# Optimization experiments

Measured on AMD Instinct MI355X. Metric: run time of the kernel, lower is better.

The kernel has to match this reference:

```python
import jax, jax.numpy as jnp
import numpy as np

BATCH, L, E = 8192, 4096, 12  # E = log2(L) butterfly stages


def setup_inputs() -> dict:
    key = jax.random.key(0)
    kx, kw = jax.random.split(key)
    x = jax.random.normal(kx, (BATCH, L), dtype=jnp.float32)
    # Stacked per-stage weights: stage s has an (L, 2) coefficient table
    # (matches nn.Parameter(torch.randn(L, 2)) for each of E stages).
    W = jax.random.normal(kw, (E, L, 2), dtype=jnp.float32)
    return {"x": x, "W": W}


def _butterfly(x, W):
    # rightmost=True: apply the smallest-stride factor first (stride 1 -> L/2).
    B = x.shape[0]
    e = W.shape[0]
    y = x
    for s in range(e):
        d = 1 << s                      # pairing stride at this stage
        g = L // (2 * d)                # number of butterfly groups
        yr = y.reshape(B, g, 2, d)      # pairs (i, i ^ d) along last dim
        Wr = W[s].reshape(g, 2, d, 2)   # per-row 2x2 mix coefficients
        top, bot = yr[:, :, 0, :], yr[:, :, 1, :]
        new_top = Wr[:, 0, :, 0] * top + Wr[:, 0, :, 1] * bot
        new_bot = Wr[:, 1, :, 0] * bot + Wr[:, 1, :, 1] * top
        y = jnp.stack([new_top, new_bot], axis=2).reshape(B, L)
    return y


def reference(x, W):
    return _butterfly(x, W)
```

## Files before the change

### kernel.cpp

```cpp
#include <hip/hip_runtime.h>


constexpr int LROW = 4096;
constexpr int RPB  = 4;
constexpr int NBLK = 8192 / RPB;

__device__ __forceinline__ int slotf(int P3, int P2, int P1, int P0) {
    const int b012 = (P0 ^ P1 ^ P2) & 7;
    const int b3   = (P1 ^ (P2 >> 1)) & 1;
    const int U    = (P3 << 5) | (P2 << 2) | (P1 >> 1);
    return (U << 4) | (b3 << 3) | b012;
}

template<int S>
__device__ __forceinline__ void loadA(float2 (&w)[8], const float* __restrict__ W, int t) {
    const float4* q4 = reinterpret_cast<const float4*>(W + (size_t)S * 8192 + 16 * t);
    #pragma unroll
    for (int m = 0; m < 4; ++m) {
        const float4 q = q4[m];
        w[2*m]   = make_float2(q.x, q.y);
        w[2*m+1] = make_float2(q.z, q.w);
    }
}

template<int S, int STEP>
__device__ __forceinline__ void loadG(float2 (&w)[8], const float* __restrict__ W, int pbase) {
    const float2* q2 = reinterpret_cast<const float2*>(W) + (size_t)S * 4096 + pbase;
    #pragma unroll
    for (int m = 0; m < 8; ++m) w[m] = q2[m * STEP];
}

template<int DL>
__device__ __forceinline__ void stage(float (&v)[RPB][8], const float2 (&w)[8]) {
    #pragma unroll
    for (int g = 0; g < 8; g += 2*DL)
        #pragma unroll
        for (int m = 0; m < DL; ++m) {
            const int a = g + m, c = a + DL;
            #pragma unroll
            for (int r = 0; r < RPB; ++r) {
                const float va = v[r][a], vb = v[r][c];
                v[r][a] = w[a].x * va + w[a].y * vb;
                v[r][c] = w[c].x * vb + w[c].y * va;
            }
        }
}

__global__ __launch_bounds__(512)
void butterfly12_kernel(const float* __restrict__ x,
                        const float* __restrict__ W,
                        float* __restrict__ out)
{
    __shared__ float2 lds[6144];

    const int t  = threadIdx.x;
    const int t6 = t >> 6;
    const int t3 = (t >> 3) & 7;
    const int t0 = t & 7;
    const size_t row0 = (size_t)blockIdx.x * RPB;

    float v[RPB][8];
    float2 wbA[8], wbB[8];

    #pragma unroll
    for (int r = 0; r < RPB; ++r) {
        const float4* xr = reinterpret_cast<const float4*>(x + (row0 + r) * LROW + 8 * t);
        const float4 qa = xr[0], qb = xr[1];
        v[r][0]=qa.x; v[r][1]=qa.y; v[r][2]=qa.z; v[r][3]=qa.w;
        v[r][4]=qb.x; v[r][5]=qb.y; v[r][6]=qb.z; v[r][7]=qb.w;
    }

    const int pB = t6*512 + t3*64 + t0;
    const int pC = t6*512 + t3*8  + t0;

    loadA<0>(wbA, W, t);
    loadA<1>(wbB, W, t);
    stage<1>(v, wbA);
    loadA<2>(wbA, W, t);
    stage<2>(v, wbB);
    loadG<3, 8>(wbB, W, pB);
    stage<4>(v, wbA);

    #pragma unroll
    for (int h = 0; h < 2; ++h) {
        asm volatile("" ::: "memory");
        #pragma unroll
        for (int i = 0; i < 8; ++i)
            lds[slotf(t6, t3, t0, i)] = make_float2(v[2*h][i], v[2*h+1][i]);
        asm volatile("s_waitcnt lgkmcnt(0)" ::: "memory");
        __builtin_amdgcn_sched_barrier(0);
        #pragma unroll
        for (int j = 0; j < 8; ++j) {
            const float2 q = lds[slotf(t6, t3, j, t0)];
            v[2*h][j] = q.x; v[2*h+1][j] = q.y;
        }
    }

    loadG<4, 8>(wbA, W, pB);
    stage<1>(v, wbB);
    loadG<5, 8>(wbB, W, pB);
    stage<2>(v, wbA);
    loadG<6, 64>(wbA, W, pC);
    stage<4>(v, wbB);

    #pragma unroll
    for (int h = 0; h < 2; ++h) {
        asm volatile("" ::: "memory");
        #pragma unroll
        for (int j = 0; j < 8; ++j)
            lds[slotf(t6, t3, j, t0)] = make_float2(v[2*h][j], v[2*h+1][j]);
        asm volatile("s_waitcnt lgkmcnt(0)" ::: "memory");
        __builtin_amdgcn_sched_barrier(0);
        #pragma unroll
        for (int k = 0; k < 8; ++k) {
            const float2 q = lds[slotf(t6, k, t3, t0)];
            v[2*h][k] = q.x; v[2*h+1][k] = q.y;
        }
    }

    loadG<7, 64>(wbB, W, pC);
    stage<1>(v, wbA);
    loadG<8, 64>(wbA, W, pC);
    stage<2>(v, wbB);
    loadG<9, 512>(wbB, W, t);
    stage<4>(v, wbA);

    {
        #pragma unroll
        for (int k = 0; k < 8; ++k)
            lds[slotf(t6, k, t3, t0)] = make_float2(v[0][k], v[1][k]);
        __syncthreads();
        #pragma unroll
        for (int m = 0; m < 8; ++m) {
            const float2 q = lds[slotf(m, t6, t3, t0)];
            v[0][m] = q.x; v[1][m] = q.y;
        }
        __syncthreads();
        #pragma unroll
        for (int k = 0; k < 8; ++k)
            lds[slotf(t6, k, t3, t0)] = make_float2(v[2][k], v[3][k]);
        __syncthreads();
        #pragma unroll
        for (int m = 0; m < 8; ++m) {
            const float2 q = lds[slotf(m, t6, t3, t0)];
            v[2][m] = q.x; v[3][m] = q.y;
        }
    }

    loadG<10, 512>(wbA, W, t);
    stage<1>(v, wbB);
    loadG<11, 512>(wbB, W, t);
    stage<2>(v, wbA);
    stage<4>(v, wbB);

    #pragma unroll
    for (int r = 0; r < RPB; ++r) {
        float* orow = out + (row0 + r) * LROW;
        #pragma unroll
        for (int m = 0; m < 8; ++m)
            orow[m*512 + t] = v[r][m];
    }
}

extern "C" void kernel_launch(void* const* d_in, const int* in_sizes, int n_in,
                              void* d_out, int out_size, void* d_ws, size_t ws_size,
                              hipStream_t stream) {
    const float* x = (const float*)d_in[0];
    const float* W = (const float*)d_in[1];
    float* out = (float*)d_out;

    butterfly12_kernel<<<NBLK, 512, 0, stream>>>(x, W, out);
}
```

Measured before the change: 268.3 us.

## Process four row groups per block with software-prefetched next-group loads

Each block now handles four groups of four rows sequentially, prefetching the next group's x rows into a second register set while computing the current group. The block count drops by a factor of four. The double-buffered weight loads are replaced by per-stage scoped loads. A __syncthreads is added before LDS reuse across groups. This is meant to hide global load latency behind compute, but it raises register pressure (two v arrays) and reduces the number of blocks and so the parallelism across CUs.

```diff
diff --git a/kernel.cpp b/kernel.cpp
--- a/kernel.cpp
+++ b/kernel.cpp
@@ -3,7 +3,8 @@
 
 constexpr int LROW = 4096;
 constexpr int RPB  = 4;
-constexpr int NBLK = 8192 / RPB;
+constexpr int GPB  = 4;
+constexpr int NBLK = 8192 / (RPB * GPB);
 
 __device__ __forceinline__ int slotf(int P3, int P2, int P1, int P0) {
     const int b012 = (P0 ^ P1 ^ P2) & 7;
@@ -46,22 +47,8 @@
         }
 }
 
-__global__ __launch_bounds__(512)
-void butterfly12_kernel(const float* __restrict__ x,
-                        const float* __restrict__ W,
-                        float* __restrict__ out)
-{
-    __shared__ float2 lds[6144];
-
-    const int t  = threadIdx.x;
-    const int t6 = t >> 6;
-    const int t3 = (t >> 3) & 7;
-    const int t0 = t & 7;
-    const size_t row0 = (size_t)blockIdx.x * RPB;
-
-    float v[RPB][8];
-    float2 wbA[8], wbB[8];
-
+__device__ __forceinline__ void loadX(float (&v)[RPB][8], const float* __restrict__ x,
+                                      size_t row0, int t) {
     #pragma unroll
     for (int r = 0; r < RPB; ++r) {
         const float4* xr = reinterpret_cast<const float4*>(x + (row0 + r) * LROW + 8 * t);
@@ -69,17 +56,27 @@
         v[r][0]=qa.x; v[r][1]=qa.y; v[r][2]=qa.z; v[r][3]=qa.w;
         v[r][4]=qb.x; v[r][5]=qb.y; v[r][6]=qb.z; v[r][7]=qb.w;
     }
+}
+
+template<bool PF>
+__device__ __forceinline__ void group_body(float (&v)[RPB][8], float (&vn)[RPB][8],
+                                           const float* __restrict__ x,
+                                           const float* __restrict__ W,
+                                           float* __restrict__ out,
+                                           size_t row0, size_t row0n,
+                                           int t, int t6, int t3, int t0,
+                                           float2* lds)
+{
+    if (PF) loadX(vn, x, row0n, t);
 
     const int pB = t6*512 + t3*64 + t0;
     const int pC = t6*512 + t3*8  + t0;
 
-    loadA<0>(wbA, W, t);
-    loadA<1>(wbB, W, t);
-    stage<1>(v, wbA);
-    loadA<2>(wbA, W, t);
-    stage<2>(v, wbB);
-    loadG<3, 8>(wbB, W, pB);
-    stage<4>(v, wbA);
+    { float2 w[8]; loadA<0>(w, W, t); stage<1>(v, w); }
+    { float2 w[8]; loadA<1>(w, W, t); stage<2>(v, w); }
+    { float2 w[8]; loadA<2>(w, W, t); stage<4>(v, w); }
+
+    __syncthreads();
 
     #pragma unroll
     for (int h = 0; h < 2; ++h) {
@@ -96,12 +93,9 @@
         }
     }
 
-    loadG<4, 8>(wbA, W, pB);
-    stage<1>(v, wbB);
-    loadG<5, 8>(wbB, W, pB);
-    stage<2>(v, wbA);
-    loadG<6, 64>(wbA, W, pC);
-    stage<4>(v, wbB);
+    { float2 w[8]; loadG<3, 8>(w, W, pB); stage<1>(v, w); }
+    { float2 w[8]; loadG<4, 8>(w, W, pB); stage<2>(v, w); }
+    { float2 w[8]; loadG<5, 8>(w, W, pB); stage<4>(v, w); }
 
     #pragma unroll
     for (int h = 0; h < 2; ++h) {
@@ -118,12 +112,9 @@
         }
     }
 
-    loadG<7, 64>(wbB, W, pC);
-    stage<1>(v, wbA);
-    loadG<8, 64>(wbA, W, pC);
-    stage<2>(v, wbB);
-    loadG<9, 512>(wbB, W, t);
-    stage<4>(v, wbA);
+    { float2 w[8]; loadG<6, 64>(w, W, pC); stage<1>(v, w); }
+    { float2 w[8]; loadG<7, 64>(w, W, pC); stage<2>(v, w); }
+    { float2 w[8]; loadG<8, 64>(w, W, pC); stage<4>(v, w); }
 
     {
         #pragma unroll
@@ -147,11 +138,9 @@
         }
     }
 
-    loadG<10, 512>(wbA, W, t);
-    stage<1>(v, wbB);
-    loadG<11, 512>(wbB, W, t);
-    stage<2>(v, wbA);
-    stage<4>(v, wbB);
+    { float2 w[8]; loadG<9,  512>(w, W, t); stage<1>(v, w); }
+    { float2 w[8]; loadG<10, 512>(w, W, t); stage<2>(v, w); }
+    { float2 w[8]; loadG<11, 512>(w, W, t); stage<4>(v, w); }
 
     #pragma unroll
     for (int r = 0; r < RPB; ++r) {
@@ -160,6 +149,29 @@
         for (int m = 0; m < 8; ++m)
             orow[m*512 + t] = v[r][m];
     }
+}
+
+__global__ __launch_bounds__(512)
+void butterfly12_kernel(const float* __restrict__ x,
+                        const float* __restrict__ W,
+                        float* __restrict__ out)
+{
+    __shared__ float2 lds[8192];
+
+    const int t  = threadIdx.x;
+    const int t6 = t >> 6;
+    const int t3 = (t >> 3) & 7;
+    const int t0 = t & 7;
+    const size_t rowbase = (size_t)blockIdx.x * (RPB * GPB);
+
+    float vA[RPB][8], vB[RPB][8];
+
+    loadX(vA, x, rowbase, t);
+
+    group_body<true >(vA, vB, x, W, out, rowbase + 0*RPB, rowbase + 1*RPB, t, t6, t3, t0, lds);
+    group_body<true >(vB, vA, x, W, out, rowbase + 1*RPB, rowbase + 2*RPB, t, t6, t3, t0, lds);
+    group_body<true >(vA, vB, x, W, out, rowbase + 2*RPB, rowbase + 3*RPB, t, t6, t3, t0, lds);
+    group_body<false>(vB, vA, x, W, out, rowbase + 3*RPB, rowbase + 3*RPB, t, t6, t3, t0, lds);
 }
 
 extern "C" void kernel_launch(void* const* d_in, const int* in_sizes, int n_in,
```

Measured after the change: 278.6 us. +3.8%, slower.

## Replace LDS transposes for middle stages with cross-lane swizzle exchanges

Applied to the files above, without the earlier changes.

Stages 3-8 now exchange partner values between lanes of the same wavefront using ds_swizzle (strides 1-16) and ds_bpermute (stride 32), replacing two LDS round-trip transposes. A single swizzled float4 LDS transpose, guarded by one barrier, redistributes data for the last three stages. The aim is to cut LDS traffic and barriers and to use coalesced weight loads. In exchange, every element now costs a cross-lane op at each of six stages and the multiply work roughly doubles, because each lane computes its own output.

```diff
diff --git a/kernel.cpp b/kernel.cpp
--- a/kernel.cpp
+++ b/kernel.cpp
@@ -5,11 +5,19 @@
 constexpr int RPB  = 4;
 constexpr int NBLK = 8192 / RPB;
 
-__device__ __forceinline__ int slotf(int P3, int P2, int P1, int P0) {
-    const int b012 = (P0 ^ P1 ^ P2) & 7;
-    const int b3   = (P1 ^ (P2 >> 1)) & 1;
-    const int U    = (P3 << 5) | (P2 << 2) | (P1 >> 1);
-    return (U << 4) | (b3 << 3) | b012;
+__device__ __forceinline__ int swz(int s) { return s ^ ((s >> 6) & 7); }
+
+template<int D>
+__device__ __forceinline__ float xl(float x, int bpa) {
+    const int xi = __builtin_bit_cast(int, x);
+    int r;
+    if      constexpr (D == 1)  r = __builtin_amdgcn_ds_swizzle(xi, 0x041F);
+    else if constexpr (D == 2)  r = __builtin_amdgcn_ds_swizzle(xi, 0x081F);
+    else if constexpr (D == 4)  r = __builtin_amdgcn_ds_swizzle(xi, 0x101F);
+    else if constexpr (D == 8)  r = __builtin_amdgcn_ds_swizzle(xi, 0x201F);
+    else if constexpr (D == 16) r = __builtin_amdgcn_ds_swizzle(xi, 0x401F);
+    else                        r = __builtin_amdgcn_ds_bpermute(bpa, xi);
+    return __builtin_bit_cast(float, r);
 }
 
 template<int S>
@@ -23,15 +31,15 @@
     }
 }
 
-template<int S, int STEP>
-__device__ __forceinline__ void loadG(float2 (&w)[8], const float* __restrict__ W, int pbase) {
-    const float2* q2 = reinterpret_cast<const float2*>(W) + (size_t)S * 4096 + pbase;
+template<int S>
+__device__ __forceinline__ void loadD(float2 (&w)[8], const float* __restrict__ W, int t) {
+    const float2* q2 = reinterpret_cast<const float2*>(W) + (size_t)S * 4096 + t;
     #pragma unroll
-    for (int m = 0; m < 8; ++m) w[m] = q2[m * STEP];
+    for (int m = 0; m < 8; ++m) w[m] = q2[m * 512];
 }
 
 template<int DL>
-__device__ __forceinline__ void stage(float (&v)[RPB][8], const float2 (&w)[8]) {
+__device__ __forceinline__ void rstage(float (&v)[RPB][8], const float2 (&w)[8]) {
     #pragma unroll
     for (int g = 0; g < 8; g += 2*DL)
         #pragma unroll
@@ -46,21 +54,33 @@
         }
 }
 
+template<int S, int D>
+__device__ __forceinline__ void xstage(float (&v)[RPB][8], const float* __restrict__ W,
+                                       int t, int bpa) {
+    float2 w[8];
+    loadA<S>(w, W, t);
+    #pragma unroll
+    for (int r = 0; r < RPB; ++r) {
+        float u[8];
+        #pragma unroll
+        for (int i = 0; i < 8; ++i) u[i] = xl<D>(v[r][i], bpa);
+        #pragma unroll
+        for (int i = 0; i < 8; ++i) v[r][i] = w[i].x * v[r][i] + w[i].y * u[i];
+    }
+}
+
 __global__ __launch_bounds__(512)
 void butterfly12_kernel(const float* __restrict__ x,
                         const float* __restrict__ W,
                         float* __restrict__ out)
 {
-    __shared__ float2 lds[6144];
+    __shared__ float4 lds4[4096];
 
-    const int t  = threadIdx.x;
-    const int t6 = t >> 6;
-    const int t3 = (t >> 3) & 7;
-    const int t0 = t & 7;
+    const int t   = threadIdx.x;
+    const int bpa = ((t & 63) ^ 32) << 2;
     const size_t row0 = (size_t)blockIdx.x * RPB;
 
     float v[RPB][8];
-    float2 wbA[8], wbB[8];
 
     #pragma unroll
     for (int r = 0; r < RPB; ++r) {
@@ -70,95 +90,37 @@
         v[r][4]=qb.x; v[r][5]=qb.y; v[r][6]=qb.z; v[r][7]=qb.w;
     }
 
-    const int pB = t6*512 + t3*64 + t0;
-    const int pC = t6*512 + t3*8  + t0;
+    { float2 w[8]; loadA<0>(w, W, t); rstage<1>(v, w); }
+    { float2 w[8]; loadA<1>(w, W, t); rstage<2>(v, w); }
+    { float2 w[8]; loadA<2>(w, W, t); rstage<4>(v, w); }
 
-    loadA<0>(wbA, W, t);
-    loadA<1>(wbB, W, t);
-    stage<1>(v, wbA);
-    loadA<2>(wbA, W, t);
-    stage<2>(v, wbB);
-    loadG<3, 8>(wbB, W, pB);
-    stage<4>(v, wbA);
+    xstage<3, 1 >(v, W, t, bpa);
+    xstage<4, 2 >(v, W, t, bpa);
+    xstage<5, 4 >(v, W, t, bpa);
+    xstage<6, 8 >(v, W, t, bpa);
+    xstage<7, 16>(v, W, t, bpa);
+    xstage<8, 32>(v, W, t, bpa);
 
     #pragma unroll
-    for (int h = 0; h < 2; ++h) {
-        asm volatile("" ::: "memory");
-        #pragma unroll
-        for (int i = 0; i < 8; ++i)
-            lds[slotf(t6, t3, t0, i)] = make_float2(v[2*h][i], v[2*h+1][i]);
-        asm volatile("s_waitcnt lgkmcnt(0)" ::: "memory");
-        __builtin_amdgcn_sched_barrier(0);
-        #pragma unroll
-        for (int j = 0; j < 8; ++j) {
-            const float2 q = lds[slotf(t6, t3, j, t0)];
-            v[2*h][j] = q.x; v[2*h+1][j] = q.y;
-        }
+    for (int i = 0; i < 8; ++i)
+        lds4[swz(8*t + i)] = make_float4(v[0][i], v[1][i], v[2][i], v[3][i]);
+    __syncthreads();
+    #pragma unroll
+    for (int k = 0; k < 8; ++k) {
+        const float4 q = lds4[swz(512*k + t)];
+        v[0][k] = q.x; v[1][k] = q.y; v[2][k] = q.z; v[3][k] = q.w;
     }
 
-    loadG<4, 8>(wbA, W, pB);
-    stage<1>(v, wbB);
-    loadG<5, 8>(wbB, W, pB);
-    stage<2>(v, wbA);
-    loadG<6, 64>(wbA, W, pC);
-    stage<4>(v, wbB);
-
-    #pragma unroll
-    for (int h = 0; h < 2; ++h) {
-        asm volatile("" ::: "memory");
-        #pragma unroll
-        for (int j = 0; j < 8; ++j)
-            lds[slotf(t6, t3, j, t0)] = make_float2(v[2*h][j], v[2*h+1][j]);
-        asm volatile("s_waitcnt lgkmcnt(0)" ::: "memory");
-        __builtin_amdgcn_sched_barrier(0);
-        #pragma unroll
-        for (int k = 0; k < 8; ++k) {
-            const float2 q = lds[slotf(t6, k, t3, t0)];
-            v[2*h][k] = q.x; v[2*h+1][k] = q.y;
-        }
-    }
-
-    loadG<7, 64>(wbB, W, pC);
-    stage<1>(v, wbA);
-    loadG<8, 64>(wbA, W, pC);
-    stage<2>(v, wbB);
-    loadG<9, 512>(wbB, W, t);
-    stage<4>(v, wbA);
-
-    {
-        #pragma unroll
-        for (int k = 0; k < 8; ++k)
-            lds[slotf(t6, k, t3, t0)] = make_float2(v[0][k], v[1][k]);
-        __syncthreads();
-        #pragma unroll
-        for (int m = 0; m < 8; ++m) {
-            const float2 q = lds[slotf(m, t6, t3, t0)];
-            v[0][m] = q.x; v[1][m] = q.y;
-        }
-        __syncthreads();
-        #pragma unroll
-        for (int k = 0; k < 8; ++k)
-            lds[slotf(t6, k, t3, t0)] = make_float2(v[2][k], v[3][k]);
-        __syncthreads();
-        #pragma unroll
-        for (int m = 0; m < 8; ++m) {
-            const float2 q = lds[slotf(m, t6, t3, t0)];
-            v[2][m] = q.x; v[3][m] = q.y;
-        }
-    }
-
-    loadG<10, 512>(wbA, W, t);
-    stage<1>(v, wbB);
-    loadG<11, 512>(wbB, W, t);
-    stage<2>(v, wbA);
-    stage<4>(v, wbB);
+    { float2 w[8]; loadD<9 >(w, W, t); rstage<1>(v, w); }
+    { float2 w[8]; loadD<10>(w, W, t); rstage<2>(v, w); }
+    { float2 w[8]; loadD<11>(w, W, t); rstage<4>(v, w); }
 
     #pragma unroll
     for (int r = 0; r < RPB; ++r) {
         float* orow = out + (row0 + r) * LROW;
         #pragma unroll
-        for (int m = 0; m < 8; ++m)
-            orow[m*512 + t] = v[r][m];
+        for (int k = 0; k < 8; ++k)
+            orow[k*512 + t] = v[r][k];
     }
 }
 
```

Result: slower. 285.5 us (+6.4%).
